# Performance work log

Measured on AMD Instinct MI355X. Metric: run time of the kernel, lower is better.

## Reference

```python
import jax, jax.numpy as jnp
import numpy as np

DIM = 1024
HEADS = 8
DIM_HEAD = 64
HIDDEN = HEADS * DIM_HEAD  # 512
SCALE = DIM_HEAD ** -0.5
BATCH = 16384
EPS = 1e-12  # F.normalize eps


def setup_inputs() -> dict:
    key = jax.random.key(0)
    k0, k1, k2 = jax.random.split(key, 3)
    x = jax.random.normal(k0, (BATCH, DIM), dtype=jnp.float32)
    w_qkv = jax.random.normal(k1, (3 * HIDDEN, DIM), dtype=jnp.float32) * 0.02
    w_out = jax.random.normal(k2, (DIM, HIDDEN), dtype=jnp.float32) * 0.02
    b_out = jnp.zeros((DIM,), dtype=jnp.float32)
    g = jnp.ones((1, DIM), dtype=jnp.float32)
    return {"x": x, "w_qkv": w_qkv, "w_out": w_out, "b_out": b_out, "g": g}


def reference(x, w_qkv, w_out, b_out, g):
    b = x.shape[0]
    # Conv1d(kernel=1, no bias) on n=1 sequence == matmul with (3*hidden, dim) weight
    qkv = x @ w_qkv.T  # (b, 3*hidden)
    q, k, v = jnp.split(qkv, 3, axis=1)  # each (b, hidden)
    # rearrange 'b (h c) n -> b h c n' with n=1 -> (b, h, c)
    q = q.reshape(b, HEADS, DIM_HEAD)
    k = k.reshape(b, HEADS, DIM_HEAD)
    v = v.reshape(b, HEADS, DIM_HEAD)
    # q.softmax(dim=-2) is over the c axis
    q = jax.nn.softmax(q, axis=-1) * SCALE
    # k.softmax(dim=-1) is over the n axis of size 1 -> all ones (kept faithful)
    k = jax.nn.softmax(k[..., None], axis=-1)[..., 0]
    # context = einsum('bhdn,bhen->bhde', k, v); out = einsum('bhde,bhdn->bhen', context, q)
    # with n=1 this collapses to out_e = (sum_d k_d q_d) * v_e; fused to avoid (b,h,d,e)
    s = jnp.einsum('bhd,bhd->bh', k, q)  # (b, h)
    out = s[..., None] * v  # (b, h, e)
    out = out.reshape(b, HIDDEN)  # 'b h c n -> b (h c) n', squeeze(-1)
    # Linear(hidden, dim)
    out = out @ w_out.T + b_out  # (b, dim)
    # RMSNorm_MLP: F.normalize(x, dim=1) * g * sqrt(dim)
    norm = jnp.linalg.norm(out, axis=1, keepdims=True)
    out = out / jnp.maximum(norm, EPS) * g * jnp.sqrt(jnp.float32(DIM))
    return out
```

## Files before the change

kernel.cpp:

```cpp
#include <hip/hip_runtime.h>
#include <hip/hip_bf16.h>


typedef __attribute__((ext_vector_type(8))) short bf16x8;
typedef __attribute__((ext_vector_type(4))) float f32x4;

struct alignas(16) bfvec8 { __hip_bfloat16 h[8]; };
struct alignas(8)  bfvec4 { __hip_bfloat16 h[4]; };

__device__ __forceinline__ bfvec8 pack8(float4 a, float4 b) {
    bfvec8 o;
    o.h[0] = __float2bfloat16(a.x); o.h[1] = __float2bfloat16(a.y);
    o.h[2] = __float2bfloat16(a.z); o.h[3] = __float2bfloat16(a.w);
    o.h[4] = __float2bfloat16(b.x); o.h[5] = __float2bfloat16(b.y);
    o.h[6] = __float2bfloat16(b.z); o.h[7] = __float2bfloat16(b.w);
    return o;
}

__device__ __forceinline__ bfvec4 pack4(float4 a) {
    bfvec4 o;
    o.h[0] = __float2bfloat16(a.x); o.h[1] = __float2bfloat16(a.y);
    o.h[2] = __float2bfloat16(a.z); o.h[3] = __float2bfloat16(a.w);
    return o;
}

__global__ __launch_bounds__(256)
void weff_only(const float* __restrict__ Wo, const float* __restrict__ Wv,
               __hip_bfloat16* __restrict__ Weff) {
    __shared__ __align__(16) __hip_bfloat16 As[64 * 32];
    __shared__ __align__(16) __hip_bfloat16 Bs[64 * 32];
    __shared__ __align__(16) float Bf[32 * 65];

    const int tid  = threadIdx.x;
    const int lane = tid & 63;
    const int wave = tid >> 6;
    const int wm   = wave >> 1;
    const int wn   = wave & 1;
    const int quad = lane >> 4;
    const int tr   = lane & 15;
    const int m0   = (blockIdx.x >> 4) * 64;
    const int n0   = (blockIdx.x & 15) * 64;

    f32x4 acc[2][2];
#pragma unroll
    for (int i = 0; i < 2; ++i)
#pragma unroll
        for (int j = 0; j < 2; ++j)
            acc[i][j] = (f32x4){0.f, 0.f, 0.f, 0.f};

    for (int kt = 0; kt < 512; kt += 32) {
        {
            int r = tid >> 2, c = tid & 3;
            int s = (r >> 1) & 3;
            int kg = (c ^ s) << 3;
            const float* sp = Wo + (size_t)(m0 + r) * 512 + kt + kg;
            float4 a = *(const float4*)sp, b = *(const float4*)(sp + 4);
            *(bfvec8*)(As + r * 32 + (c << 3)) = pack8(a, b);
        }
        {
            int kr = tid >> 3, c8 = (tid & 7) << 3;
            const float* sp = Wv + (size_t)(kt + kr) * 1024 + n0 + c8;
            float4 a = *(const float4*)sp, b = *(const float4*)(sp + 4);
            *(float4*)(Bf + kr * 65 + c8)     = a;
            *(float4*)(Bf + kr * 65 + c8 + 4) = b;
        }
        __syncthreads();
        {
            int n = tid >> 2, cc = tid & 3, k8 = cc << 3;
            float4 a, b;
            a.x = Bf[(k8 + 0) * 65 + n]; a.y = Bf[(k8 + 1) * 65 + n];
            a.z = Bf[(k8 + 2) * 65 + n]; a.w = Bf[(k8 + 3) * 65 + n];
            b.x = Bf[(k8 + 4) * 65 + n]; b.y = Bf[(k8 + 5) * 65 + n];
            b.z = Bf[(k8 + 6) * 65 + n]; b.w = Bf[(k8 + 7) * 65 + n];
            int cs = cc ^ ((n >> 1) & 3);
            *(bfvec8*)(Bs + n * 32 + cs * 8) = pack8(a, b);
        }
        __syncthreads();

        bf16x8 af[2], bfr[2];
#pragma unroll
        for (int mi = 0; mi < 2; ++mi) {
            int r = wm * 32 + mi * 16 + tr;
            int c = quad ^ ((r >> 1) & 3);
            af[mi] = *(const bf16x8*)(As + r * 32 + c * 8);
        }
#pragma unroll
        for (int ni = 0; ni < 2; ++ni) {
            int r = wn * 32 + ni * 16 + tr;
            int c = quad ^ ((r >> 1) & 3);
            bfr[ni] = *(const bf16x8*)(Bs + r * 32 + c * 8);
        }
#pragma unroll
        for (int mi = 0; mi < 2; ++mi)
#pragma unroll
            for (int ni = 0; ni < 2; ++ni)
                acc[mi][ni] = __builtin_amdgcn_mfma_f32_16x16x32_bf16(
                    af[mi], bfr[ni], acc[mi][ni], 0, 0, 0);
        __syncthreads();
    }

#pragma unroll
    for (int mi = 0; mi < 2; ++mi)
#pragma unroll
        for (int ni = 0; ni < 2; ++ni) {
            const int col = n0 + wn * 32 + ni * 16 + tr;
#pragma unroll
            for (int r = 0; r < 4; ++r) {
                const int row = m0 + wm * 32 + mi * 16 + quad * 4 + r;
                Weff[(size_t)row * 1024 + col] =
                    __float2bfloat16(acc[mi][ni][r] * 0.125f);
            }
        }
}


#define GLL(gp, lp) __builtin_amdgcn_global_load_lds( \
    (const __attribute__((address_space(1))) void*)(gp), \
    (__attribute__((address_space(3))) void*)(lp), 16, 0, 0)

__global__ __launch_bounds__(512, 2)
void main_fused(const float* __restrict__ X,
                const __hip_bfloat16* __restrict__ W,
                const float* __restrict__ bias,
                const float* __restrict__ g,
                float* __restrict__ out) {
    __shared__ __align__(16) __hip_bfloat16 sm[69632];
    __shared__ float wpart[8][64];
    __shared__ float scrow[64];

    const int tid  = threadIdx.x;
    const int lane = tid & 63;
    const int wc   = tid >> 6;
    const int quad = lane >> 4;
    const int tr   = lane & 15;

    const int m0 = blockIdx.x * 64;

    const int ra = tid >> 3, q = tid & 7;
    const int aq = (((q >> 1) ^ (ra & 3)) << 3) + (q & 1) * 4;
    const float* Ag = X + (size_t)(m0 + ra) * 1024 + aq;
    const int AdsW = tid * 4;

    const int brow = tid >> 2;
    const int kswz = (((tid & 3) ^ (brow & 3)) << 3);

    const int ac = ((quad ^ (tr & 3)) << 3);

    f32x4 acc[4][8];
#pragma unroll
    for (int mi = 0; mi < 4; ++mi)
#pragma unroll
        for (int ni = 0; ni < 8; ++ni)
            acc[mi][ni] = (f32x4){0.f, 0.f, 0.f, 0.f};

    {
#pragma unroll
        for (int i = 0; i < 4; ++i)
            GLL(W + (size_t)(i * 128 + brow) * 1024 + kswz,
                sm + 4096 + (i * 512 + tid) * 8);
        float4 pav = *(const float4*)Ag;
#pragma unroll
        for (int i = 4; i < 8; ++i)
            GLL(W + (size_t)(i * 128 + brow) * 1024 + kswz,
                sm + 4096 + (i * 512 + tid) * 8);
        asm volatile("s_waitcnt vmcnt(4)" ::: "memory");
        *(bfvec4*)(sm + AdsW) = pack4(pav);
        asm volatile("s_waitcnt vmcnt(0) lgkmcnt(0)" ::: "memory");
        __builtin_amdgcn_s_barrier();
    }

#define TILE(U, RB) do { \
    const int u_ = (U); \
    float4 pav; \
    if (u_ < 31) { \
        const int kt_ = (u_ + 1) * 32; \
        _Pragma("unroll") \
        for (int i = 0; i < 4; ++i) \
            GLL(W + (size_t)(i * 128 + brow) * 1024 + kt_ + kswz, \
                sm + 4096 + ((RB) ^ 1) * 32768 + (i * 512 + tid) * 8); \
        pav = *(const float4*)(Ag + kt_); \
        _Pragma("unroll") \
        for (int i = 4; i < 8; ++i) \
            GLL(W + (size_t)(i * 128 + brow) * 1024 + kt_ + kswz, \
                sm + 4096 + ((RB) ^ 1) * 32768 + (i * 512 + tid) * 8); \
    } \
    bf16x8 af[4], bfr[8]; \
    _Pragma("unroll") \
    for (int mi = 0; mi < 4; ++mi) \
        af[mi] = *(const bf16x8*)(sm + (RB) * 2048 + (mi * 16 + tr) * 32 + ac); \
    _Pragma("unroll") \
    for (int ni = 0; ni < 8; ++ni) \
        bfr[ni] = *(const bf16x8*)(sm + 4096 + (RB) * 32768 + \
                                   (wc * 128 + ni * 16 + tr) * 32 + ac); \
    asm volatile("s_waitcnt lgkmcnt(0)" ::: "memory"); \
    __builtin_amdgcn_sched_barrier(0); \
    __builtin_amdgcn_s_setprio(1); \
    _Pragma("unroll") \
    for (int mi = 0; mi < 4; ++mi) \
        _Pragma("unroll") \
        for (int ni = 0; ni < 8; ++ni) \
            acc[mi][ni] = __builtin_amdgcn_mfma_f32_16x16x32_bf16( \
                af[mi], bfr[ni], acc[mi][ni], 0, 0, 0); \
    __builtin_amdgcn_s_setprio(0); \
    if (u_ < 31) { \
        asm volatile("s_waitcnt vmcnt(4)" ::: "memory"); \
        *(bfvec4*)(sm + ((RB) ^ 1) * 2048 + AdsW) = pack4(pav); \
    } \
    asm volatile("s_waitcnt vmcnt(0) lgkmcnt(0)" ::: "memory"); \
    __builtin_amdgcn_s_barrier(); \
} while (0)

    for (int it = 0; it < 16; ++it) {
        TILE(it * 2,     0);
        TILE(it * 2 + 1, 1);
    }
#undef TILE

    float bvv[8], gvv[8];
    int coln[8];
#pragma unroll
    for (int ni = 0; ni < 8; ++ni) {
        coln[ni] = wc * 128 + ni * 16 + tr;
        bvv[ni] = bias[coln[ni]];
        gvv[ni] = g[coln[ni]];
    }

#pragma unroll
    for (int mi = 0; mi < 4; ++mi)
#pragma unroll
        for (int rr = 0; rr < 4; ++rr) {
            float p = 0.f;
#pragma unroll
            for (int ni = 0; ni < 8; ++ni) {
                const float t = acc[mi][ni][rr] + bvv[ni];
                acc[mi][ni][rr] = t;
                p += t * t;
            }
#pragma unroll
            for (int msk = 1; msk < 16; msk <<= 1)
                p += __shfl_xor(p, msk, 64);
            if (tr == 0) wpart[wc][mi * 16 + quad * 4 + rr] = p;
        }
    __syncthreads();

    if (tid < 64) {
        float s = 0.f;
#pragma unroll
        for (int w = 0; w < 8; ++w) s += wpart[w][tid];
        scrow[tid] = 32.0f / fmaxf(sqrtf(s), 1e-12f);
    }
    __syncthreads();

#pragma unroll
    for (int mi = 0; mi < 4; ++mi)
#pragma unroll
        for (int rr = 0; rr < 4; ++rr) {
            const int r16 = mi * 16 + quad * 4 + rr;
            const float sc = scrow[r16];
#pragma unroll
            for (int ni = 0; ni < 8; ++ni)
                out[(size_t)(m0 + r16) * 1024 + coln[ni]] =
                    acc[mi][ni][rr] * sc * gvv[ni];
        }
}

extern "C" void kernel_launch(void* const* d_in, const int* in_sizes, int n_in,
                              void* d_out, int out_size, void* d_ws, size_t ws_size,
                              hipStream_t stream) {
    const float* x     = (const float*)d_in[0];
    const float* w_qkv = (const float*)d_in[1];
    const float* w_out = (const float*)d_in[2];
    const float* b_out = (const float*)d_in[3];
    const float* g     = (const float*)d_in[4];

    const int D = 1024, H = 512;
    const float* wv = w_qkv + (size_t)2 * H * D;

    __hip_bfloat16* weff_bf = (__hip_bfloat16*)d_ws;

    weff_only<<<256, 256, 0, stream>>>(w_out, wv, weff_bf);
    main_fused<<<256, 512, 0, stream>>>(x, weff_bf, b_out, g, (float*)d_out);
}
```

Before: 179.6 us.

## Load weight fragments directly from global into registers, drop LDS staging for W

Each wave now reads its 128-column slice of the bf16 effective weight straight from global memory into register fragments, double-buffered across k-steps. Only the converted X tile still goes through LDS. This removes the large LDS buffer, the global-to-LDS copies for W and the LDS fragment reads for W. In exchange it uses many more VGPRs, so launch bounds drop to one block per SIMD set, and the global reads are less coalesced with no sharing of W across waves inside the block.

```diff
diff --git a/kernel.cpp b/kernel.cpp
--- a/kernel.cpp
+++ b/kernel.cpp
@@ -6,7 +6,6 @@
 typedef __attribute__((ext_vector_type(4))) float f32x4;
 
 struct alignas(16) bfvec8 { __hip_bfloat16 h[8]; };
-struct alignas(8)  bfvec4 { __hip_bfloat16 h[4]; };
 
 __device__ __forceinline__ bfvec8 pack8(float4 a, float4 b) {
     bfvec8 o;
@@ -14,13 +13,6 @@
     o.h[2] = __float2bfloat16(a.z); o.h[3] = __float2bfloat16(a.w);
     o.h[4] = __float2bfloat16(b.x); o.h[5] = __float2bfloat16(b.y);
     o.h[6] = __float2bfloat16(b.z); o.h[7] = __float2bfloat16(b.w);
-    return o;
-}
-
-__device__ __forceinline__ bfvec4 pack4(float4 a) {
-    bfvec4 o;
-    o.h[0] = __float2bfloat16(a.x); o.h[1] = __float2bfloat16(a.y);
-    o.h[2] = __float2bfloat16(a.z); o.h[3] = __float2bfloat16(a.w);
     return o;
 }
 
@@ -113,18 +105,13 @@
         }
 }
 
-
-#define GLL(gp, lp) __builtin_amdgcn_global_load_lds( \
-    (const __attribute__((address_space(1))) void*)(gp), \
-    (__attribute__((address_space(3))) void*)(lp), 16, 0, 0)
-
-__global__ __launch_bounds__(512, 2)
+__global__ __launch_bounds__(512, 1)
 void main_fused(const float* __restrict__ X,
                 const __hip_bfloat16* __restrict__ W,
                 const float* __restrict__ bias,
                 const float* __restrict__ g,
                 float* __restrict__ out) {
-    __shared__ __align__(16) __hip_bfloat16 sm[69632];
+    __shared__ __align__(16) __hip_bfloat16 Asm[2][2048];
     __shared__ float wpart[8][64];
     __shared__ float scrow[64];
 
@@ -133,18 +120,20 @@
     const int wc   = tid >> 6;
     const int quad = lane >> 4;
     const int tr   = lane & 15;
-
-    const int m0 = blockIdx.x * 64;
-
-    const int ra = tid >> 3, q = tid & 7;
-    const int aq = (((q >> 1) ^ (ra & 3)) << 3) + (q & 1) * 4;
-    const float* Ag = X + (size_t)(m0 + ra) * 1024 + aq;
-    const int AdsW = tid * 4;
-
-    const int brow = tid >> 2;
-    const int kswz = (((tid & 3) ^ (brow & 3)) << 3);
-
-    const int ac = ((quad ^ (tr & 3)) << 3);
+    const int m0   = blockIdx.x * 64;
+
+    const int arow = tid >> 2;
+    const int akq  = (tid & 3) ^ ((tid >> 3) & 3);
+    const float* Agp = X + (size_t)(m0 + arow) * 1024 + akq * 8;
+
+    int aoff[4];
+#pragma unroll
+    for (int mi = 0; mi < 4; ++mi) {
+        const int row = mi * 16 + tr;
+        aoff[mi] = (row * 4 + (quad ^ ((row >> 1) & 3))) * 8;
+    }
+
+    const __hip_bfloat16* Wb = W + (size_t)(wc * 128 + tr) * 1024 + quad * 8;
 
     f32x4 acc[4][8];
 #pragma unroll
@@ -153,68 +142,56 @@
         for (int ni = 0; ni < 8; ++ni)
             acc[mi][ni] = (f32x4){0.f, 0.f, 0.f, 0.f};
 
-    {
-#pragma unroll
-        for (int i = 0; i < 4; ++i)
-            GLL(W + (size_t)(i * 128 + brow) * 1024 + kswz,
-                sm + 4096 + (i * 512 + tid) * 8);
-        float4 pav = *(const float4*)Ag;
-#pragma unroll
-        for (int i = 4; i < 8; ++i)
-            GLL(W + (size_t)(i * 128 + brow) * 1024 + kswz,
-                sm + 4096 + (i * 512 + tid) * 8);
-        asm volatile("s_waitcnt vmcnt(4)" ::: "memory");
-        *(bfvec4*)(sm + AdsW) = pack4(pav);
-        asm volatile("s_waitcnt vmcnt(0) lgkmcnt(0)" ::: "memory");
-        __builtin_amdgcn_s_barrier();
-    }
-
-#define TILE(U, RB) do { \
+    float4 pa0, pa1;
+    bf16x8 b0[8], b1[8], af[4];
+
+    if (tid < 256) {
+        pa0 = *(const float4*)Agp;
+        pa1 = *(const float4*)(Agp + 4);
+    }
+#pragma unroll
+    for (int ni = 0; ni < 8; ++ni)
+        b0[ni] = *(const bf16x8*)(Wb + ni * 16384);
+    if (tid < 256)
+        *(bfvec8*)(&Asm[0][tid * 8]) = pack8(pa0, pa1);
+    __syncthreads();
+
+#define BODY(U, P, BC, BN) do { \
     const int u_ = (U); \
-    float4 pav; \
     if (u_ < 31) { \
-        const int kt_ = (u_ + 1) * 32; \
+        if (tid < 256) { \
+            pa0 = *(const float4*)(Agp + (u_ + 1) * 32); \
+            pa1 = *(const float4*)(Agp + (u_ + 1) * 32 + 4); \
+        } \
         _Pragma("unroll") \
-        for (int i = 0; i < 4; ++i) \
-            GLL(W + (size_t)(i * 128 + brow) * 1024 + kt_ + kswz, \
-                sm + 4096 + ((RB) ^ 1) * 32768 + (i * 512 + tid) * 8); \
-        pav = *(const float4*)(Ag + kt_); \
-        _Pragma("unroll") \
-        for (int i = 4; i < 8; ++i) \
-            GLL(W + (size_t)(i * 128 + brow) * 1024 + kt_ + kswz, \
-                sm + 4096 + ((RB) ^ 1) * 32768 + (i * 512 + tid) * 8); \
+        for (int ni = 0; ni < 8; ++ni) \
+            BN[ni] = *(const bf16x8*)(Wb + ni * 16384 + (u_ + 1) * 32); \
     } \
-    bf16x8 af[4], bfr[8]; \
     _Pragma("unroll") \
     for (int mi = 0; mi < 4; ++mi) \
-        af[mi] = *(const bf16x8*)(sm + (RB) * 2048 + (mi * 16 + tr) * 32 + ac); \
-    _Pragma("unroll") \
-    for (int ni = 0; ni < 8; ++ni) \
-        bfr[ni] = *(const bf16x8*)(sm + 4096 + (RB) * 32768 + \
-                                   (wc * 128 + ni * 16 + tr) * 32 + ac); \
-    asm volatile("s_waitcnt lgkmcnt(0)" ::: "memory"); \
-    __builtin_amdgcn_sched_barrier(0); \
+        af[mi] = *(const bf16x8*)(&Asm[P][aoff[mi]]); \
     __builtin_amdgcn_s_setprio(1); \
     _Pragma("unroll") \
     for (int mi = 0; mi < 4; ++mi) \
         _Pragma("unroll") \
         for (int ni = 0; ni < 8; ++ni) \
             acc[mi][ni] = __builtin_amdgcn_mfma_f32_16x16x32_bf16( \
-                af[mi], bfr[ni], acc[mi][ni], 0, 0, 0); \
+                af[mi], BC[ni], acc[mi][ni], 0, 0, 0); \
     __builtin_amdgcn_s_setprio(0); \
     if (u_ < 31) { \
-        asm volatile("s_waitcnt vmcnt(4)" ::: "memory"); \
-        *(bfvec4*)(sm + ((RB) ^ 1) * 2048 + AdsW) = pack4(pav); \
+        if (tid < 256) \
+            *(bfvec8*)(&Asm[(P) ^ 1][tid * 8]) = pack8(pa0, pa1); \
+        asm volatile("s_waitcnt lgkmcnt(0)" ::: "memory"); \
+        __builtin_amdgcn_s_barrier(); \
+        __builtin_amdgcn_sched_barrier(0); \
     } \
-    asm volatile("s_waitcnt vmcnt(0) lgkmcnt(0)" ::: "memory"); \
-    __builtin_amdgcn_s_barrier(); \
 } while (0)
 
     for (int it = 0; it < 16; ++it) {
-        TILE(it * 2,     0);
-        TILE(it * 2 + 1, 1);
-    }
-#undef TILE
+        BODY(it * 2,     0, b0, b1);
+        BODY(it * 2 + 1, 1, b1, b0);
+    }
+#undef BODY
 
     float bvv[8], gvv[8];
     int coln[8];
```

Result: slower. 192.6 us (+7.2%).
